# Kernel tuning notes

Measured on AMD Instinct MI355X. Metric: run time of the kernel, lower is better.

## Reference

```python
import jax, jax.numpy as jnp
import numpy as np
import math

L = 4096
D = 1280
H = 16
HD = D // H  # 80
NSEG = 4


def setup_inputs() -> dict:
    key = jax.random.key(0)
    ks = jax.random.split(key, 8)
    x = jax.random.normal(ks[0], (L, D), dtype=jnp.float32)
    cu_seqlens = jnp.array([0, 1024, 2048, 3072, 4096], dtype=jnp.int32)
    rotary_pos_emb = jax.random.uniform(ks[1], (L, HD // 2), dtype=jnp.float32) * (2 * math.pi)
    s = 1.0 / math.sqrt(D)
    W_qkv = jax.random.normal(ks[2], (3 * D, D), dtype=jnp.float32) * s
    b_qkv = jax.random.normal(ks[3], (3 * D,), dtype=jnp.float32) * 0.01
    W_proj = jax.random.normal(ks[4], (D, D), dtype=jnp.float32) * s
    b_proj = jax.random.normal(ks[5], (D,), dtype=jnp.float32) * 0.01
    return {"x": x, "cu_seqlens": cu_seqlens, "rotary_pos_emb": rotary_pos_emb,
            "W_qkv": W_qkv, "b_qkv": b_qkv, "W_proj": W_proj, "b_proj": b_proj}


def _rotary_half(t):
    t1, t2 = jnp.split(t, 2, axis=-1)
    return jnp.concatenate([-t2, t1], axis=-1)


def _apply_rope(t, freq):
    # t: (L, H, HD), freq: (L, HD/2)
    cos = jnp.concatenate([jnp.cos(freq), jnp.cos(freq)], axis=-1)[:, None, :]
    sin = jnp.concatenate([jnp.sin(freq), jnp.sin(freq)], axis=-1)[:, None, :]
    return t * cos + _rotary_half(t) * sin


def reference(x, cu_seqlens, rotary_pos_emb, W_qkv, b_qkv, W_proj, b_proj):
    seq_len = x.shape[0]
    qkv = (x @ W_qkv.T + b_qkv).reshape(seq_len, 3, H, HD)
    q, k, v = qkv[:, 0], qkv[:, 1], qkv[:, 2]  # each (L, H, HD)
    q = _apply_rope(q, rotary_pos_emb)
    k = _apply_rope(k, rotary_pos_emb)
    # scores: (H, L, L)
    scores = jnp.einsum('lhd,mhd->hlm', q, k) / math.sqrt(HD)
    # block-diagonal mask from cu_seqlens: same segment -> 0, else finfo.min
    seg = jnp.searchsorted(cu_seqlens, jnp.arange(seq_len, dtype=jnp.int32), side='right')  # (L,)
    same = seg[:, None] == seg[None, :]
    neg = jnp.finfo(scores.dtype).min
    scores = scores + jnp.where(same, jnp.array(0.0, scores.dtype), neg)[None, :, :]
    attn = jax.nn.softmax(scores.astype(jnp.float32), axis=-1).astype(q.dtype)
    out = jnp.einsum('hlm,mhd->lhd', attn, v).reshape(seq_len, D)
    return out @ W_proj.T + b_proj
```

## Files before the change

### kernel.cpp

```cpp
#include <hip/hip_runtime.h>
#include <hip/hip_bf16.h>
#include <math.h>

#define LL   4096
#define DD   1280
#define HH   16
#define HDD  80
#define QKVN (3 * DD)

typedef __attribute__((ext_vector_type(8))) short sv8;
typedef __attribute__((ext_vector_type(4))) short sv4;
typedef __attribute__((ext_vector_type(4))) float fv4;

#if __has_builtin(__builtin_amdgcn_mfma_f32_16x16x16bf16_1k)
#define MFMA16(a, b, c) __builtin_amdgcn_mfma_f32_16x16x16bf16_1k(a, b, c, 0, 0, 0)
#elif __has_builtin(__builtin_amdgcn_mfma_f32_16x16x16_bf16)
#define MFMA16(a, b, c) __builtin_amdgcn_mfma_f32_16x16x16_bf16(a, b, c, 0, 0, 0)
#else
__device__ static inline fv4 MFMA16(sv4, sv4, fv4 c) { return c; }
#endif

static __device__ __forceinline__ unsigned short f2bf(float f) {
  unsigned int u = __builtin_bit_cast(unsigned int, f);
  u += 0x7FFF + ((u >> 16) & 1);
  return (unsigned short)(u >> 16);
}
static __device__ __forceinline__ float bf2f(unsigned short b) {
  unsigned int u = ((unsigned int)b) << 16;
  return __builtin_bit_cast(float, u);
}
static __device__ __forceinline__ unsigned int cvt_pk_bf16(float lo, float hi) {
  __hip_bfloat162 h = __float22bfloat162_rn(make_float2(lo, hi));
  unsigned int u;
  __builtin_memcpy(&u, &h, 4);
  return u;
}

#define GLD_LDS(gsrc, ldst)                                                          \
  __builtin_amdgcn_global_load_lds(                                                  \
      (const __attribute__((address_space(1))) unsigned int*)(gsrc),                 \
      (__attribute__((address_space(3))) unsigned int*)(ldst), 16, 0, 0)

__global__ __launch_bounds__(256) void cast3_kernel(
    const float* __restrict__ x, const float* __restrict__ w1,
    const float* __restrict__ w2, unsigned short* __restrict__ xb,
    unsigned short* __restrict__ w1b, unsigned short* __restrict__ w2b) {
  const int n0 = LL * DD / 8, n1 = QKVN * DD / 8, n2 = DD * DD / 8;
  int i = blockIdx.x * 256 + threadIdx.x;
  const float* in; unsigned short* out; int j;
  if (i < n0)           { in = x;  out = xb;  j = i; }
  else if (i < n0 + n1) { in = w1; out = w1b; j = i - n0; }
  else if (i < n0 + n1 + n2) { in = w2; out = w2b; j = i - n0 - n1; }
  else return;
  const float4* p = (const float4*)(in + (size_t)j * 8);
  float4 v0 = p[0], v1 = p[1];
  union { sv8 v; unsigned int u[4]; } o;
  o.u[0] = cvt_pk_bf16(v0.x, v0.y);
  o.u[1] = cvt_pk_bf16(v0.z, v0.w);
  o.u[2] = cvt_pk_bf16(v1.x, v1.y);
  o.u[3] = cvt_pk_bf16(v1.z, v1.w);
  *(sv8*)(out + (size_t)j * 8) = o.v;
}

__global__ __launch_bounds__(256) void gemm_bf16_kernel(
    const unsigned short* __restrict__ A, const unsigned short* __restrict__ B,
    const float* __restrict__ bias, void* __restrict__ Cv,
    int M, int N, int K, int out_bf16) {
  __shared__ __attribute__((aligned(16))) unsigned short As[2][128 * 64];
  __shared__ __attribute__((aligned(16))) unsigned short Bs[2][128 * 64];
  int tid = threadIdx.x, w = tid >> 6, lane = tid & 63;
  int g = lane >> 4, l15 = lane & 15;
  int wr = w >> 1, wc = w & 1;
  int bm = blockIdx.y * 128, bn = blockIdx.x * 128;

  fv4 acc[4][4];
#pragma unroll
  for (int a = 0; a < 4; ++a)
#pragma unroll
    for (int b = 0; b < 4; ++b) acc[a][b] = (fv4){0.f, 0.f, 0.f, 0.f};

  auto STAGE = [&](int buf, int k0) {
#pragma unroll
    for (int i = 0; i < 4; ++i) {
      int c = w * 4 + i;
      int row = 8 * c + (lane >> 3);
      int cb = lane & 7;
      int gcol = k0 + ((cb ^ (row & 7)) * 8);
      GLD_LDS(A + (size_t)(bm + row) * K + gcol, As[buf] + c * 512);
      GLD_LDS(B + (size_t)(bn + row) * K + gcol, Bs[buf] + c * 512);
    }
  };

  int nt = K / 64, cur = 0;
  STAGE(0, 0);
  if (nt > 1) STAGE(1, 64);
  for (int t = 0; t < nt; ++t) {
    if (t + 1 < nt) asm volatile("s_waitcnt vmcnt(8)" ::: "memory");
    else            asm volatile("s_waitcnt vmcnt(0)" ::: "memory");
    __builtin_amdgcn_sched_barrier(0);
    asm volatile("s_barrier" ::: "memory");
    const unsigned short* Ab = As[cur];
    const unsigned short* Bb = Bs[cur];
#pragma unroll
    for (int s = 0; s < 2; ++s) {
      sv8 af[4], bf[4];
#pragma unroll
      for (int t4 = 0; t4 < 4; ++t4) {
        int ra = wr * 64 + t4 * 16 + l15;
        af[t4] = *(const sv8*)(Ab + ra * 64 + (((s * 4 + g) ^ (ra & 7)) * 8));
        int rb = wc * 64 + t4 * 16 + l15;
        bf[t4] = *(const sv8*)(Bb + rb * 64 + (((s * 4 + g) ^ (rb & 7)) * 8));
      }
#pragma unroll
      for (int mt = 0; mt < 4; ++mt)
#pragma unroll
        for (int nt2 = 0; nt2 < 4; ++nt2)
          acc[mt][nt2] = __builtin_amdgcn_mfma_f32_16x16x32_bf16(af[mt], bf[nt2], acc[mt][nt2], 0, 0, 0);
    }
    asm volatile("s_waitcnt lgkmcnt(0)" ::: "memory");
    asm volatile("s_barrier" ::: "memory");
    if (t + 2 < nt) STAGE(cur, (t + 2) * 64);
    cur ^= 1;
  }

  if (out_bf16) {
    unsigned short* C = (unsigned short*)Cv;
#pragma unroll
    for (int mt = 0; mt < 4; ++mt)
#pragma unroll
      for (int nt2 = 0; nt2 < 4; ++nt2)
#pragma unroll
        for (int r = 0; r < 4; ++r) {
          int m = bm + wr * 64 + mt * 16 + 4 * g + r;
          int n = bn + wc * 64 + nt2 * 16 + l15;
          C[(size_t)m * N + n] = f2bf(acc[mt][nt2][r] + bias[n]);
        }
  } else {
    float* C = (float*)Cv;
#pragma unroll
    for (int mt = 0; mt < 4; ++mt)
#pragma unroll
      for (int nt2 = 0; nt2 < 4; ++nt2)
#pragma unroll
        for (int r = 0; r < 4; ++r) {
          int m = bm + wr * 64 + mt * 16 + 4 * g + r;
          int n = bn + wc * 64 + nt2 * 16 + l15;
          C[(size_t)m * N + n] = acc[mt][nt2][r] + bias[n];
        }
  }
}

__global__ __launch_bounds__(192) void pack_qk_kernel(
    const unsigned short* __restrict__ qkvb, const float* __restrict__ freqs,
    unsigned short* __restrict__ Qb, unsigned short* __restrict__ Kb) {
  int l = blockIdx.x;
  __shared__ float cs[40], sn[40];
  if (threadIdx.x < 40) {
    float f = freqs[(size_t)l * 40 + threadIdx.x];
    cs[threadIdx.x] = cosf(f);
    sn[threadIdx.x] = sinf(f);
  }
  __syncthreads();
  int t = threadIdx.x;
  if (t >= 160) return;
  int which = t / 80;
  int rem   = t % 80;
  int h = rem / 5, pg = rem % 5;
  int d0 = pg * 8;
  const unsigned short* src = qkvb + (size_t)l * QKVN + which * DD + h * HDD;
  union { sv8 v; unsigned short u[8]; } A, B;
  A.v = *(const sv8*)(src + d0);
  B.v = *(const sv8*)(src + d0 + 40);
  float scale = which ? 1.0f : 0.16129822676f;
  float lo[8], hi[8];
#pragma unroll
  for (int j = 0; j < 8; ++j) {
    float c = cs[d0 + j], s = sn[d0 + j];
    float a = bf2f(A.u[j]), b = bf2f(B.u[j]);
    lo[j] = (a * c - b * s) * scale;
    hi[j] = (b * c + a * s) * scale;
  }
  union { sv8 v; unsigned int u[4]; } OL, OH;
#pragma unroll
  for (int j = 0; j < 4; ++j) {
    OL.u[j] = cvt_pk_bf16(lo[2 * j], lo[2 * j + 1]);
    OH.u[j] = cvt_pk_bf16(hi[2 * j], hi[2 * j + 1]);
  }
  unsigned short* dst = (which ? Kb : Qb) + ((size_t)h * LL + l) * HDD;
  *(sv8*)(dst + d0) = OL.v;
  *(sv8*)(dst + d0 + 40) = OH.v;
}

__global__ __launch_bounds__(256) void pack_v_kernel(
    const unsigned short* __restrict__ qkvb, unsigned short* __restrict__ Vt) {
  __shared__ unsigned short vb[HDD][66];
  int l0 = blockIdx.x * 64, h = blockIdx.y;
  for (int idx = threadIdx.x; idx < 64 * HDD; idx += 256) {
    int l = idx / HDD, d = idx % HDD;
    vb[d][l] = qkvb[(size_t)(l0 + l) * QKVN + 2 * DD + h * HDD + d];
  }
  __syncthreads();
  for (int idx = threadIdx.x; idx < 64 * HDD; idx += 256) {
    int d = idx >> 6, l = idx & 63;
    Vt[((size_t)h * HDD + d) * LL + l0 + l] = vb[d][l];
  }
}

__global__ __launch_bounds__(256) void attn_mfma_kernel(
    const unsigned short* __restrict__ Qb,
    const unsigned short* __restrict__ Kb,
    const unsigned short* __restrict__ Vt,
    const int* __restrict__ cu,
    unsigned short* __restrict__ outb) {
  __shared__ __attribute__((aligned(16))) unsigned short Ks[2][64 * HDD];
  __shared__ __attribute__((aligned(16))) unsigned short Vl[2][HDD * 64];
  int tid = threadIdx.x, w = tid >> 6, lane = tid & 63;
  int g = lane >> 4, l15 = lane & 15;

  int bid = blockIdx.x;
  int sw = (bid & 7) * 128 + (bid >> 3);
  int h = sw >> 6;
  int q0 = (sw & 63) * 64;

  int s0 = 0, s1 = LL;
#pragma unroll
  for (int i = 0; i < 4; ++i) {
    int a = cu[i], b = cu[i + 1];
    if (q0 >= a && q0 < b) { s0 = a; s1 = b; }
  }

  int qrow = q0 + w * 16 + l15;
  const unsigned short* qp = Qb + ((size_t)h * LL + qrow) * HDD;
  sv8 aq[2];
#pragma unroll
  for (int s = 0; s < 2; ++s) aq[s] = *(const sv8*)(qp + s * 32 + g * 8);
  union { sv4 v; uint2 u2; } qt;
  qt.u2 = *(const uint2*)(qp + 64 + 4 * g);

  auto STAGE = [&](int buf, int kb) {
#pragma unroll
    for (int i = 0; i < 5; ++i) {
      int cid = w + 4 * i;
      if (cid < 10) {
        int B = cid * 1024 + (lane << 4);
        int row = B / 160;
        int gran = (B % 160) >> 4;
        int sgran = (gran < 8) ? (gran ^ (row & 7)) : gran;
        GLD_LDS(Kb + ((size_t)h * LL + kb + row) * HDD + sgran * 8,
                Ks[buf] + cid * 512);
      } else {
        int c = cid - 10;
        int d = 8 * c + (lane >> 3);
        int cb = lane & 7;
        GLD_LDS(Vt + ((size_t)h * HDD + d) * LL + kb + ((cb ^ (d & 7)) * 8),
                Vl[buf] + c * 512);
      }
    }
  };

  fv4 o[5];
#pragma unroll
  for (int dt = 0; dt < 5; ++dt) o[dt] = (fv4){0.f, 0.f, 0.f, 0.f};
  float lsum = 0.f;

  int cur = 0;
  STAGE(0, s0);
  if (s0 + 64 < s1) STAGE(1, s0 + 64);
  for (int kb = s0; kb < s1; kb += 64) {
    if (kb + 64 < s1) asm volatile("s_waitcnt vmcnt(5)" ::: "memory");
    else              asm volatile("s_waitcnt vmcnt(0)" ::: "memory");
    __builtin_amdgcn_sched_barrier(0);
    asm volatile("s_barrier" ::: "memory");
    const unsigned short* Kc = Ks[cur];
    const unsigned short* Vc = Vl[cur];

    fv4 sf[4];
#pragma unroll
    for (int nt = 0; nt < 4; ++nt) sf[nt] = (fv4){0.f, 0.f, 0.f, 0.f};
#pragma unroll
    for (int s = 0; s < 2; ++s) {
#pragma unroll
      for (int nt = 0; nt < 4; ++nt) {
        int key = nt * 16 + l15;
        sv8 ak = *(const sv8*)(Kc + key * HDD + (((s * 4 + g) ^ (key & 7)) * 8));
        sf[nt] = __builtin_amdgcn_mfma_f32_16x16x32_bf16(ak, aq[s], sf[nt], 0, 0, 0);
      }
    }
#pragma unroll
    for (int nt = 0; nt < 4; ++nt) {
      int key = nt * 16 + l15;
      sv4 akt = *(const sv4*)(Kc + key * HDD + (8 + (g >> 1)) * 8 + (g & 1) * 4);
      sf[nt] = MFMA16(akt, qt.v, sf[nt]);
    }

#pragma unroll
    for (int nt = 0; nt < 4; ++nt) {
      float p0 = exp2f(sf[nt][0]);
      float p1 = exp2f(sf[nt][1]);
      float p2 = exp2f(sf[nt][2]);
      float p3 = exp2f(sf[nt][3]);
      lsum += (p0 + p1) + (p2 + p3);
      union { sv4 v; unsigned int u[2]; } pa;
      pa.u[0] = cvt_pk_bf16(p0, p1);
      pa.u[1] = cvt_pk_bf16(p2, p3);
#pragma unroll
      for (int dt = 0; dt < 5; ++dt) {
        int d = dt * 16 + l15;
        sv4 vb4 = *(const sv4*)(Vc + d * 64 + (((2 * nt + (g >> 1)) ^ (d & 7)) * 8) + (g & 1) * 4);
        o[dt] = MFMA16(pa.v, vb4, o[dt]);
      }
    }
    asm volatile("s_waitcnt lgkmcnt(0)" ::: "memory");
    asm volatile("s_barrier" ::: "memory");
    if (kb + 128 < s1) STAGE(cur, kb + 128);
    cur ^= 1;
  }

  lsum += __shfl_xor(lsum, 16);
  lsum += __shfl_xor(lsum, 32);
  float inv = 1.f / lsum;
#pragma unroll
  for (int r = 0; r < 4; ++r) {
    float invr = __shfl(inv, 4 * g + r);
    int row = q0 + w * 16 + 4 * g + r;
#pragma unroll
    for (int dt = 0; dt < 5; ++dt) {
      outb[(size_t)row * DD + h * HDD + dt * 16 + l15] = f2bf(o[dt][r] * invr);
    }
  }
}

extern "C" void kernel_launch(void* const* d_in, const int* in_sizes, int n_in,
                              void* d_out, int out_size, void* d_ws, size_t ws_size,
                              hipStream_t stream) {
  const float* x     = (const float*)d_in[0];
  const int*   cu    = (const int*)d_in[1];
  const float* rope  = (const float*)d_in[2];
  const float* Wqkv  = (const float*)d_in[3];
  const float* bqkv  = (const float*)d_in[4];
  const float* Wproj = (const float*)d_in[5];
  const float* bproj = (const float*)d_in[6];
  float* out = (float*)d_out;

  char* ws = (char*)d_ws;
  unsigned short* qkvb   = (unsigned short*)ws;
  unsigned short* attn_b = (unsigned short*)ws;
  unsigned short* xb     = (unsigned short*)(ws + 31457280);
  unsigned short* Wqkvb  = (unsigned short*)(ws + 41943040);
  unsigned short* Wprojb = (unsigned short*)(ws + 51773440);
  unsigned short* Kb     = (unsigned short*)(ws + 55050240);
  unsigned short* Vt     = (unsigned short*)(ws + 71827456);
  unsigned short* Qb     = xb;

  {
    int n8 = LL * DD / 8 + QKVN * DD / 8 + DD * DD / 8;
    cast3_kernel<<<(n8 + 255) / 256, 256, 0, stream>>>(x, Wqkv, Wproj, xb, Wqkvb, Wprojb);
  }

  gemm_bf16_kernel<<<dim3(QKVN / 128, LL / 128), 256, 0, stream>>>(
      xb, Wqkvb, bqkv, qkvb, LL, QKVN, DD, 1);

  pack_qk_kernel<<<LL, 192, 0, stream>>>(qkvb, rope, Qb, Kb);
  pack_v_kernel<<<dim3(LL / 64, HH), 256, 0, stream>>>(qkvb, Vt);

  attn_mfma_kernel<<<1024, 256, 0, stream>>>(Qb, Kb, Vt, cu, attn_b);

  gemm_bf16_kernel<<<dim3(DD / 128, LL / 128), 256, 0, stream>>>(
      attn_b, Wprojb, bproj, out, LL, DD, DD, 0);
}
```

Before: 153.9 us.

## Use 256x256-tile triple-buffered GEMM with XCD-aware block mapping for QKV projection

Replaces the 128x128-tile QKV projection GEMM with a new 512-thread kernel using 256x256 output tiles and a 3-stage LDS ring buffer fed by direct global-to-LDS loads. It uses swizzled LDS addressing and the 16x16x32 bf16 MFMA. Block IDs are remapped so neighbouring tiles land on the same XCD, which should improve L2 reuse. The goal is higher arithmetic intensity and better latency hiding for the largest GEMM. The cost is more registers and a grid of only 240 blocks, which may leave some compute units idle.

```diff
diff --git a/kernel.cpp b/kernel.cpp
--- a/kernel.cpp
+++ b/kernel.cpp
@@ -62,6 +62,90 @@
   *(sv8*)(out + (size_t)j * 8) = o.v;
 }
 
+__global__ __launch_bounds__(512, 2) void gemm256_bf16_kernel(
+    const unsigned short* __restrict__ A, const unsigned short* __restrict__ B,
+    const float* __restrict__ bias, unsigned short* __restrict__ C,
+    int M, int N, int K) {
+  __shared__ __attribute__((aligned(16))) unsigned short As[3][256 * 32];
+  __shared__ __attribute__((aligned(16))) unsigned short Bs[3][256 * 32];
+  int tid = threadIdx.x, w = tid >> 6, lane = tid & 63;
+  int g = lane >> 4, l15 = lane & 15;
+  int wr = w >> 2, wc = w & 3;
+
+  int bid = blockIdx.x;
+  int wg = (bid & 7) * 30 + (bid >> 3);
+  int bm = (wg / 15) * 256;
+  int bn = (wg % 15) * 256;
+
+  fv4 acc[8][4];
+#pragma unroll
+  for (int a = 0; a < 8; ++a)
+#pragma unroll
+    for (int b = 0; b < 4; ++b) acc[a][b] = (fv4){0.f, 0.f, 0.f, 0.f};
+
+  auto STAGE = [&](int buf, int t) {
+    int k0 = t * 32;
+#pragma unroll
+    for (int i = 0; i < 4; ++i) {
+      int cid = w * 4 + i;
+      int c = cid & 15;
+      int row = c * 16 + (lane >> 2);
+      int gsrc = (lane & 3) ^ ((row >> 1) & 3);
+      const unsigned short* src = (cid < 16)
+          ? A + (size_t)(bm + row) * K + k0 + gsrc * 8
+          : B + (size_t)(bn + row) * K + k0 + gsrc * 8;
+      unsigned short* dst = ((cid < 16) ? As[buf] : Bs[buf]) + c * 512;
+      GLD_LDS(src, dst);
+    }
+  };
+
+  const int NT = 40;
+  int r = 0;
+  STAGE(0, 0);
+  STAGE(1, 1);
+  for (int t = 0; t < NT; ++t) {
+    if (t + 1 < NT) asm volatile("s_waitcnt vmcnt(4)" ::: "memory");
+    else            asm volatile("s_waitcnt vmcnt(0)" ::: "memory");
+    __builtin_amdgcn_sched_barrier(0);
+    asm volatile("s_barrier" ::: "memory");
+    int s2 = (r == 0) ? 2 : r - 1;
+    if (t + 2 < NT) STAGE(s2, t + 2);
+
+    const unsigned short* Ab = As[r];
+    const unsigned short* Bb = Bs[r];
+    sv8 af[8], bfr[4];
+#pragma unroll
+    for (int mt = 0; mt < 8; ++mt) {
+      int row = wr * 128 + mt * 16 + l15;
+      af[mt] = *(const sv8*)(Ab + row * 32 + ((g ^ ((row >> 1) & 3)) * 8));
+    }
+#pragma unroll
+    for (int nt = 0; nt < 4; ++nt) {
+      int row = wc * 64 + nt * 16 + l15;
+      bfr[nt] = *(const sv8*)(Bb + row * 32 + ((g ^ ((row >> 1) & 3)) * 8));
+    }
+#pragma unroll
+    for (int mt = 0; mt < 8; ++mt)
+#pragma unroll
+      for (int nt = 0; nt < 4; ++nt)
+        acc[mt][nt] = __builtin_amdgcn_mfma_f32_16x16x32_bf16(af[mt], bfr[nt], acc[mt][nt], 0, 0, 0);
+    r = (r == 2) ? 0 : r + 1;
+  }
+
+#pragma unroll
+  for (int mt = 0; mt < 8; ++mt)
+#pragma unroll
+    for (int nt = 0; nt < 4; ++nt) {
+      int n = bn + wc * 64 + nt * 16 + l15;
+      float bv = bias[n];
+#pragma unroll
+      for (int rr = 0; rr < 4; ++rr) {
+        int m = bm + wr * 128 + mt * 16 + 4 * g + rr;
+        C[(size_t)m * N + n] = f2bf(acc[mt][nt][rr] + bv);
+      }
+    }
+}
+
 __global__ __launch_bounds__(256) void gemm_bf16_kernel(
     const unsigned short* __restrict__ A, const unsigned short* __restrict__ B,
     const float* __restrict__ bias, void* __restrict__ Cv,
@@ -357,8 +441,8 @@
     cast3_kernel<<<(n8 + 255) / 256, 256, 0, stream>>>(x, Wqkv, Wproj, xb, Wqkvb, Wprojb);
   }
 
-  gemm_bf16_kernel<<<dim3(QKVN / 128, LL / 128), 256, 0, stream>>>(
-      xb, Wqkvb, bqkv, qkvb, LL, QKVN, DD, 1);
+  gemm256_bf16_kernel<<<240, 512, 0, stream>>>(
+      xb, Wqkvb, bqkv, qkvb, LL, QKVN, DD);
 
   pack_qk_kernel<<<LL, 192, 0, stream>>>(qkvb, rope, Qb, Kb);
   pack_v_kernel<<<dim3(LL / 64, HH), 256, 0, stream>>>(qkvb, Vt);
```

Result: faster. 144.5 us (-6.1%).
